# Kernel tuning notes

Measured on AMD Instinct MI355X. Metric: run time of the kernel, lower is better.

## Reference

```python
import jax, jax.numpy as jnp
import numpy as np

N = 100_000      # nodes
E = 3_200_000    # edges (avg degree 32)
DIM = 512        # input feature dim
HID = 16         # GCNConv hidden dim (fixed in __init__)
C = 64           # n_classes
DROP_P = 0.5     # F.dropout default


def _gcn_conv(x, W, b, row, col, deg_inv_sqrt, n_nodes):
    """PyG GCNConv: h = x@W; out[j] += norm_ij * h[i]; out += b.
    row/col already include self-loops; deg_inv_sqrt precomputed."""
    h = x @ W                                  # [N, out]
    norm = deg_inv_sqrt[row] * deg_inv_sqrt[col]  # [E+N]
    msg = h[row] * norm[:, None]               # gather + scale
    out = jax.ops.segment_sum(msg, col, num_segments=n_nodes)
    return out + b


def setup_inputs() -> dict:
    key = jax.random.key(0)
    k = jax.random.split(key, 6)
    x = jax.random.normal(k[0], (N, DIM), dtype=jnp.float32)
    edge_index = jax.random.randint(k[1], (2, E), 0, N, dtype=jnp.int32)
    W1 = jax.random.normal(k[2], (DIM, HID), dtype=jnp.float32) * (1.0 / np.sqrt(DIM))
    b1 = jnp.zeros((HID,), dtype=jnp.float32)
    W2 = jax.random.normal(k[3], (HID, C), dtype=jnp.float32) * (1.0 / np.sqrt(HID))
    b2 = jnp.zeros((C,), dtype=jnp.float32)
    return {"x": x, "edge_index": edge_index, "W1": W1, "b1": b1, "W2": W2, "b2": b2}


def reference(x, edge_index, W1, b1, W2, b2):
    n = x.shape[0]
    loops = jnp.arange(n, dtype=edge_index.dtype)
    row = jnp.concatenate([edge_index[0], loops])  # sources (with self-loops)
    col = jnp.concatenate([edge_index[1], loops])  # targets (with self-loops)
    # symmetric normalization: deg over targets with unit edge weight
    deg = jax.ops.segment_sum(jnp.ones_like(col, dtype=x.dtype), col, num_segments=n)
    deg_inv_sqrt = jnp.where(deg > 0, jax.lax.rsqrt(deg), 0.0)

    h = jax.nn.relu(_gcn_conv(x, W1, b1, row, col, deg_inv_sqrt, n))
    # F.dropout(x) -> p=0.5, training=True; deterministic fixed key
    keep = jax.random.bernoulli(jax.random.key(42), 1.0 - DROP_P, h.shape)
    h = jnp.where(keep, h / (1.0 - DROP_P), 0.0)
    logits = _gcn_conv(h, W2, b2, row, col, deg_inv_sqrt, n)
    return jax.nn.log_softmax(logits, axis=1)
```

## Files before the change

### kernel.cpp

```cpp
#include <hip/hip_runtime.h>

#define NN    100000
#define NE    3200000
#define DIMK  512
#define HIDN  16
#define NCLS  64
#define NBUCK 391
#define NBLK  512
#define CHUNK 6250
#define BCAP  10240

__device__ __forceinline__ unsigned rotl32(unsigned x, int r){ return (x << r) | (x >> (32 - r)); }

__device__ __forceinline__ unsigned threefry_bits(unsigned i){
  const unsigned k0 = 0u, k1 = 42u;
  const unsigned k2 = 0x1BD11BDAu ^ k0 ^ k1;
  unsigned a = 0u + k0, b = i + k1;
#define TF_R(r) { a += b; b = rotl32(b, (r)); b ^= a; }
  TF_R(13) TF_R(15) TF_R(26) TF_R(6)  a += k1; b += k2 + 1u;
  TF_R(17) TF_R(29) TF_R(16) TF_R(24) a += k2; b += k0 + 2u;
  TF_R(13) TF_R(15) TF_R(26) TF_R(6)  a += k0; b += k1 + 3u;
  TF_R(17) TF_R(29) TF_R(16) TF_R(24) a += k1; b += k2 + 4u;
  TF_R(13) TF_R(15) TF_R(26) TF_R(6)  a += k2; b += k0 + 5u;
#undef TF_R
  return a ^ b;
}

__global__ __launch_bounds__(256) void kp1_hist(const int* __restrict__ col, int* __restrict__ M){
  __shared__ int h[NBUCK];
  const int blk = blockIdx.x, t = threadIdx.x;
  for (int q = t; q < NBUCK; q += 256) h[q] = 0;
  __syncthreads();
  const int e0 = blk * CHUNK;
  for (int i = t; i < CHUNK; i += 256)
    atomicAdd(&h[col[e0 + i] >> 8], 1);
  __syncthreads();
  for (int q = t; q < NBUCK; q += 256) M[blk * NBUCK + q] = h[q];
}

__global__ __launch_bounds__(512) void kp2_rowscan(int* __restrict__ M, int* __restrict__ btot){
  __shared__ int s[512];
  const int b = blockIdx.x, t = threadIdx.x;
  const int idx = t * NBUCK + b;
  int v = M[idx];
  int x = v;
  s[t] = x; __syncthreads();
  for (int d = 1; d < 512; d <<= 1){
    int y = (t >= d) ? s[t - d] : 0;
    __syncthreads();
    x += y; s[t] = x;
    __syncthreads();
  }
  M[idx] = x - v;
  if (t == 511) btot[b] = x;
}

__global__ __launch_bounds__(512) void kp2b_bscan(const int* __restrict__ btot, int* __restrict__ bbase){
  __shared__ int s[512];
  const int t = threadIdx.x;
  int v = (t < NBUCK) ? btot[t] : 0;
  int x = v;
  s[t] = x; __syncthreads();
  for (int d = 1; d < 512; d <<= 1){
    int y = (t >= d) ? s[t - d] : 0;
    __syncthreads();
    x += y; s[t] = x;
    __syncthreads();
  }
  if (t < NBUCK) bbase[t] = x - v;
  if (t == NBUCK - 1) bbase[NBUCK] = x;
}

__global__ __launch_bounds__(256) void kp3_scatter(const int* __restrict__ row, const int* __restrict__ col,
                                                   const int* __restrict__ M, const int* __restrict__ bbase,
                                                   unsigned* __restrict__ coarse){
  __shared__ int cur[NBUCK];
  const int blk = blockIdx.x, t = threadIdx.x;
  for (int q = t; q < NBUCK; q += 256) cur[q] = bbase[q] + M[blk * NBUCK + q];
  __syncthreads();
  const int e0 = blk * CHUNK;
  for (int i = t; i < CHUNK; i += 256){
    int c = col[e0 + i];
    int r = row[e0 + i];
    int p = atomicAdd(&cur[c >> 8], 1);
    coarse[p] = ((unsigned)(c & 255) << 17) | (unsigned)r;
  }
}

__global__ __launch_bounds__(1024) void kd_dis(const unsigned* __restrict__ coarse,
                                               const int* __restrict__ bbase,
                                               float* __restrict__ dis){
  __shared__ int cnt[256];
  const int b = blockIdx.x, t = threadIdx.x;
  if (t < 256) cnt[t] = 0;
  __syncthreads();
  const int base = bbase[b];
  const int nreg = bbase[b + 1] - base;
  for (int i = t; i < nreg; i += 1024)
    atomicAdd(&cnt[coarse[base + i] >> 17], 1);
  __syncthreads();
  if (t < 256){
    int n = (b << 8) + t;
    if (n < NN) dis[n] = rsqrtf((float)(cnt[t] + 1));
  }
}

__global__ __launch_bounds__(256) void k_gemm1(const float* __restrict__ x,
                                               const float* __restrict__ W1,
                                               const float* __restrict__ dis,
                                               _Float16* __restrict__ hs16){
  const int lane = threadIdx.x & 63;
  const int wid  = (blockIdx.x * blockDim.x + threadIdx.x) >> 6;
  const int nw   = (gridDim.x * blockDim.x) >> 6;
  const bool s5 = (lane & 32) != 0;
  const bool s4 = (lane & 16) != 0;
  const bool s3 = (lane & 8)  != 0;
  const bool s2 = (lane & 4)  != 0;

  float4 w4[8][4];
  const float4* W1v = (const float4*)W1;
#pragma unroll
  for (int k = 0; k < 8; ++k)
#pragma unroll
    for (int jj = 0; jj < 4; ++jj)
      w4[k][jj] = W1v[(lane * 8 + k) * 4 + jj];

  for (int n = wid; n < NN; n += nw){
    const float4* xp = (const float4*)(x + (size_t)n * DIMK + lane * 8);
    float4 xa = xp[0], xb = xp[1];
    float xv[8] = {xa.x, xa.y, xa.z, xa.w, xb.x, xb.y, xb.z, xb.w};
    float acc[16];
#pragma unroll
    for (int j = 0; j < 16; ++j) acc[j] = 0.f;
#pragma unroll
    for (int k = 0; k < 8; ++k){
      float xk = xv[k];
#pragma unroll
      for (int jj = 0; jj < 4; ++jj){
        acc[jj*4+0] = fmaf(xk, w4[k][jj].x, acc[jj*4+0]);
        acc[jj*4+1] = fmaf(xk, w4[k][jj].y, acc[jj*4+1]);
        acc[jj*4+2] = fmaf(xk, w4[k][jj].z, acc[jj*4+2]);
        acc[jj*4+3] = fmaf(xk, w4[k][jj].w, acc[jj*4+3]);
      }
    }
    float t8[8];
#pragma unroll
    for (int m = 0; m < 8; ++m){
      float keep = s5 ? acc[8+m] : acc[m];
      float give = s5 ? acc[m]   : acc[8+m];
      t8[m] = keep + __shfl_xor(give, 32, 64);
    }
    float t4[4];
#pragma unroll
    for (int m = 0; m < 4; ++m){
      float keep = s4 ? t8[4+m] : t8[m];
      float give = s4 ? t8[m]   : t8[4+m];
      t4[m] = keep + __shfl_xor(give, 16, 64);
    }
    float t2[2];
#pragma unroll
    for (int m = 0; m < 2; ++m){
      float keep = s3 ? t4[2+m] : t4[m];
      float give = s3 ? t4[m]   : t4[2+m];
      t2[m] = keep + __shfl_xor(give, 8, 64);
    }
    float keep = s2 ? t2[1] : t2[0];
    float give = s2 ? t2[0] : t2[1];
    float v = keep + __shfl_xor(give, 4, 64);
    v += __shfl_xor(v, 2, 64);
    v += __shfl_xor(v, 1, 64);
    float hv = __shfl(v, (lane & 15) * 4, 64);
    if (lane < 16) hs16[(size_t)n * HIDN + lane] = (_Float16)(hv * dis[n]);
  }
}

__global__ __launch_bounds__(1024) void k_sortagg1(const unsigned* __restrict__ coarse,
                                                   const int* __restrict__ bbase,
                                                   const _Float16* __restrict__ hs16,
                                                   const float* __restrict__ dis,
                                                   const float* __restrict__ b1,
                                                   int* __restrict__ csr,
                                                   int* __restrict__ dstart,
                                                   int* __restrict__ dcnt,
                                                   _Float16* __restrict__ h2s16){
  __shared__ int ldsCsr[BCAP];
  __shared__ int cnt[256], ofs[256], rk[256], s[256];
  const int b = blockIdx.x, t = threadIdx.x;
  const int base = bbase[b];
  const int nreg = min(bbase[b + 1] - base, BCAP);
  if (t < 256){ cnt[t] = 0; rk[t] = 0; }
  __syncthreads();
  for (int i = t; i < nreg; i += 1024)
    atomicAdd(&cnt[coarse[base + i] >> 17], 1);
  __syncthreads();
  int deg = 0, x = 0;
  if (t < 256){ deg = cnt[t]; x = deg; s[t] = x; }
  __syncthreads();
  for (int d = 1; d < 256; d <<= 1){
    int y = 0;
    if (t < 256 && t >= d) y = s[t - d];
    __syncthreads();
    if (t < 256){ x += y; s[t] = x; }
    __syncthreads();
  }
  if (t < 256) ofs[t] = x - deg;
  __syncthreads();
  for (int i = t; i < nreg; i += 1024){
    unsigned p = coarse[base + i];
    int l = p >> 17;
    int q = atomicAdd(&rk[l], 1);
    ldsCsr[ofs[l] + q] = (int)(p & 0x1FFFFu);
  }
  if (t < 256){
    int n = (b << 8) + t;
    if (n < NN){ dstart[n] = base + ofs[t]; dcnt[n] = cnt[t]; }
  }
  __syncthreads();
  for (int q = t; q < nreg; q += 1024) csr[base + q] = ldsCsr[q];
  const int g = t >> 4, j = t & 15;
  for (int d = g; d < 256; d += 64){
    const int n = (b << 8) + d;
    if (n >= NN) break;
    const int st = ofs[d], cn = cnt[d];
    float acc = 0.f;
    int i = 0;
    for (; i + 2 <= cn; i += 2){
      int r0 = ldsCsr[st + i];
      int r1 = ldsCsr[st + i + 1];
      float a0 = (float)hs16[r0 * HIDN + j];
      float a1 = (float)hs16[r1 * HIDN + j];
      acc += a0 + a1;
    }
    if (i < cn) acc += (float)hs16[ldsCsr[st + i] * HIDN + j];
    float dn = dis[n];
    float v = fmaf(dn, acc + (float)hs16[(size_t)n * HIDN + j], b1[j]);
    v = fmaxf(v, 0.f);
    unsigned bits = threefry_bits((unsigned)(n * HIDN + j));
    float kept = (bits & 0x80000000u) ? 0.f : v * 2.f;
    h2s16[(size_t)n * HIDN + j] = (_Float16)(kept * dn);
  }
}

__global__ __launch_bounds__(256) void k_agg2out(const int* __restrict__ csr,
                                                 const int* __restrict__ dstart,
                                                 const int* __restrict__ dcnt,
                                                 const _Float16* __restrict__ h2s16,
                                                 const float* __restrict__ dis,
                                                 const float* __restrict__ W2,
                                                 const float* __restrict__ b2,
                                                 float* __restrict__ out){
  const int lane = threadIdx.x & 63;
  const int wid  = (blockIdx.x * blockDim.x + threadIdx.x) >> 6;
  const int nw   = (gridDim.x * blockDim.x) >> 6;
  const int j  = lane & 15;
  const int c4 = lane >> 4;
  float wc[16];
#pragma unroll
  for (int k = 0; k < 16; ++k) wc[k] = W2[k * NCLS + lane];
  const float bb = b2[lane];
  for (int n = wid; n < NN; n += nw){
    const int start = dstart[n];
    const int end   = start + dcnt[n];
    float acc = 0.f;
    for (int base = start; base < end; base += 64){
      const int m = min(end - base, 64);
      int rv = (lane < m) ? csr[base + lane] : 0;
      const int itmax = (m + 3) >> 2;
      for (int it = 0; it < itmax; ++it){
        int e = it * 4 + c4;
        int r = __shfl(rv, e & 63, 64);
        if (e < m) acc += (float)h2s16[r * HIDN + j];
      }
    }
    acc += __shfl_xor(acc, 16, 64);
    acc += __shfl_xor(acc, 32, 64);
    float dn = dis[n];
    float aggj = dn * (acc + (float)h2s16[(size_t)n * HIDN + j]);
    float s = bb;
#pragma unroll
    for (int k = 0; k < 16; ++k) s = fmaf(__shfl(aggj, k, 64), wc[k], s);
    float m2 = s;
#pragma unroll
    for (int d = 32; d; d >>= 1) m2 = fmaxf(m2, __shfl_xor(m2, d, 64));
    float ex = __expf(s - m2);
    float sum = ex;
#pragma unroll
    for (int d = 32; d; d >>= 1) sum += __shfl_xor(sum, d, 64);
    out[(size_t)n * NCLS + lane] = (s - m2) - __logf(sum);
  }
}

extern "C" void kernel_launch(void* const* d_in, const int* in_sizes, int n_in,
                              void* d_out, int out_size, void* d_ws, size_t ws_size,
                              hipStream_t stream){
  const float* x  = (const float*)d_in[0];
  const int*   ei = (const int*)  d_in[1];
  const float* W1 = (const float*)d_in[2];
  const float* b1 = (const float*)d_in[3];
  const float* W2 = (const float*)d_in[4];
  const float* b2 = (const float*)d_in[5];
  float* out = (float*)d_out;
  const int* row = ei;
  const int* col = ei + NE;

  char* ws = (char*)d_ws;
  int*       M      = (int*)      (ws + 0);
  int*       btot   = (int*)      (ws + 800768);
  int*       bbase  = (int*)      (ws + 802368);
  int*       dstart = (int*)      (ws + 803968);
  int*       dcnt   = (int*)      (ws + 1203968);
  float*     dis    = (float*)    (ws + 1603968);
  int*       csr    = (int*)      (ws + 2003968);
  unsigned*  coarse = (unsigned*) (ws + 14803968);
  _Float16*  hs16   = (_Float16*) (ws + 27603968);
  _Float16*  h2s16  = (_Float16*) (ws + 30803968);

  kp1_hist   <<<NBLK, 256, 0, stream>>>(col, M);
  kp2_rowscan<<<NBUCK, 512, 0, stream>>>(M, btot);
  kp2b_bscan <<<1, 512, 0, stream>>>(btot, bbase);
  kp3_scatter<<<NBLK, 256, 0, stream>>>(row, col, M, bbase, coarse);
  kd_dis     <<<NBUCK, 1024, 0, stream>>>(coarse, bbase, dis);
  k_gemm1    <<<1024, 256, 0, stream>>>(x, W1, dis, hs16);
  k_sortagg1 <<<NBUCK, 1024, 0, stream>>>(coarse, bbase, hs16, dis, b1, csr, dstart, dcnt, h2s16);
  k_agg2out  <<<2048, 256, 0, stream>>>(csr, dstart, dcnt, h2s16, dis, W2, b2, out);
}
```

Baseline: 509.3 us.

## Drop global CSR; rebuild per-bucket CSR in LDS for second aggregation

Moves the degree prefix scan into the metadata kernel so dstart/dcnt are computed once. The global CSR array is no longer written. The second aggregation instead re-sorts the coarse bucket into LDS per block and aggregates there, then applies W2 and log-softmax from an LDS accumulator. This removes a 12.8MB CSR write and read, at the cost of repeating the LDS bucket sort and running the second layer with only 391 large blocks.

```diff
diff --git a/kernel.cpp b/kernel.cpp
--- a/kernel.cpp
+++ b/kernel.cpp
@@ -87,10 +87,12 @@
   }
 }
 
-__global__ __launch_bounds__(1024) void kd_dis(const unsigned* __restrict__ coarse,
-                                               const int* __restrict__ bbase,
-                                               float* __restrict__ dis){
-  __shared__ int cnt[256];
+__global__ __launch_bounds__(1024) void kd_meta(const unsigned* __restrict__ coarse,
+                                                const int* __restrict__ bbase,
+                                                int* __restrict__ dstart,
+                                                int* __restrict__ dcnt,
+                                                float* __restrict__ dis){
+  __shared__ int cnt[256], s[256];
   const int b = blockIdx.x, t = threadIdx.x;
   if (t < 256) cnt[t] = 0;
   __syncthreads();
@@ -99,9 +101,23 @@
   for (int i = t; i < nreg; i += 1024)
     atomicAdd(&cnt[coarse[base + i] >> 17], 1);
   __syncthreads();
+  int deg = 0, x = 0;
+  if (t < 256){ deg = cnt[t]; x = deg; s[t] = x; }
+  __syncthreads();
+  for (int d = 1; d < 256; d <<= 1){
+    int y = 0;
+    if (t < 256 && t >= d) y = s[t - d];
+    __syncthreads();
+    if (t < 256){ x += y; s[t] = x; }
+    __syncthreads();
+  }
   if (t < 256){
     int n = (b << 8) + t;
-    if (n < NN) dis[n] = rsqrtf((float)(cnt[t] + 1));
+    if (n < NN){
+      dstart[n] = base + (x - deg);
+      dcnt[n]   = deg;
+      dis[n]    = rsqrtf((float)(deg + 1));
+    }
   }
 }
 
@@ -176,34 +192,23 @@
 
 __global__ __launch_bounds__(1024) void k_sortagg1(const unsigned* __restrict__ coarse,
                                                    const int* __restrict__ bbase,
+                                                   const int* __restrict__ dstart,
+                                                   const int* __restrict__ dcnt,
                                                    const _Float16* __restrict__ hs16,
                                                    const float* __restrict__ dis,
                                                    const float* __restrict__ b1,
-                                                   int* __restrict__ csr,
-                                                   int* __restrict__ dstart,
-                                                   int* __restrict__ dcnt,
                                                    _Float16* __restrict__ h2s16){
   __shared__ int ldsCsr[BCAP];
-  __shared__ int cnt[256], ofs[256], rk[256], s[256];
+  __shared__ int ofs[256], cnt[256], rk[256];
   const int b = blockIdx.x, t = threadIdx.x;
   const int base = bbase[b];
   const int nreg = min(bbase[b + 1] - base, BCAP);
-  if (t < 256){ cnt[t] = 0; rk[t] = 0; }
-  __syncthreads();
-  for (int i = t; i < nreg; i += 1024)
-    atomicAdd(&cnt[coarse[base + i] >> 17], 1);
-  __syncthreads();
-  int deg = 0, x = 0;
-  if (t < 256){ deg = cnt[t]; x = deg; s[t] = x; }
-  __syncthreads();
-  for (int d = 1; d < 256; d <<= 1){
-    int y = 0;
-    if (t < 256 && t >= d) y = s[t - d];
-    __syncthreads();
-    if (t < 256){ x += y; s[t] = x; }
-    __syncthreads();
-  }
-  if (t < 256) ofs[t] = x - deg;
+  if (t < 256){
+    int n = (b << 8) + t;
+    rk[t] = 0;
+    if (n < NN){ ofs[t] = dstart[n] - base; cnt[t] = dcnt[n]; }
+    else       { ofs[t] = 0;               cnt[t] = 0; }
+  }
   __syncthreads();
   for (int i = t; i < nreg; i += 1024){
     unsigned p = coarse[base + i];
@@ -211,12 +216,7 @@
     int q = atomicAdd(&rk[l], 1);
     ldsCsr[ofs[l] + q] = (int)(p & 0x1FFFFu);
   }
-  if (t < 256){
-    int n = (b << 8) + t;
-    if (n < NN){ dstart[n] = base + ofs[t]; dcnt[n] = cnt[t]; }
-  }
-  __syncthreads();
-  for (int q = t; q < nreg; q += 1024) csr[base + q] = ldsCsr[q];
+  __syncthreads();
   const int g = t >> 4, j = t & 15;
   for (int d = g; d < 256; d += 64){
     const int n = (b << 8) + d;
@@ -241,51 +241,73 @@
   }
 }
 
-__global__ __launch_bounds__(256) void k_agg2out(const int* __restrict__ csr,
-                                                 const int* __restrict__ dstart,
-                                                 const int* __restrict__ dcnt,
-                                                 const _Float16* __restrict__ h2s16,
-                                                 const float* __restrict__ dis,
-                                                 const float* __restrict__ W2,
-                                                 const float* __restrict__ b2,
-                                                 float* __restrict__ out){
-  const int lane = threadIdx.x & 63;
-  const int wid  = (blockIdx.x * blockDim.x + threadIdx.x) >> 6;
-  const int nw   = (gridDim.x * blockDim.x) >> 6;
-  const int j  = lane & 15;
-  const int c4 = lane >> 4;
+__global__ __launch_bounds__(1024) void k_agg2b(const unsigned* __restrict__ coarse,
+                                                const int* __restrict__ bbase,
+                                                const int* __restrict__ dstart,
+                                                const int* __restrict__ dcnt,
+                                                const _Float16* __restrict__ h2s16,
+                                                const float* __restrict__ dis,
+                                                const float* __restrict__ W2,
+                                                const float* __restrict__ b2,
+                                                float* __restrict__ out){
+  __shared__ int ldsCsr[BCAP];
+  __shared__ int ofs[256], cnt[256], rk[256];
+  __shared__ float accT[256 * HIDN];
+  const int b = blockIdx.x, t = threadIdx.x;
+  const int base = bbase[b];
+  const int nreg = min(bbase[b + 1] - base, BCAP);
+  if (t < 256){
+    int n = (b << 8) + t;
+    rk[t] = 0;
+    if (n < NN){ ofs[t] = dstart[n] - base; cnt[t] = dcnt[n]; }
+    else       { ofs[t] = 0;               cnt[t] = 0; }
+  }
+  __syncthreads();
+  for (int i = t; i < nreg; i += 1024){
+    unsigned p = coarse[base + i];
+    int l = p >> 17;
+    int q = atomicAdd(&rk[l], 1);
+    ldsCsr[ofs[l] + q] = (int)(p & 0x1FFFFu);
+  }
+  __syncthreads();
+  const int g = t >> 4, j = t & 15;
+  for (int d = g; d < 256; d += 64){
+    const int n = (b << 8) + d;
+    float acc = 0.f;
+    if (n < NN){
+      const int st = ofs[d], cn = cnt[d];
+      int i = 0;
+      for (; i + 2 <= cn; i += 2){
+        int r0 = ldsCsr[st + i];
+        int r1 = ldsCsr[st + i + 1];
+        acc += (float)h2s16[r0 * HIDN + j] + (float)h2s16[r1 * HIDN + j];
+      }
+      if (i < cn) acc += (float)h2s16[ldsCsr[st + i] * HIDN + j];
+    }
+    accT[d * HIDN + j] = acc;
+  }
+  __syncthreads();
+  const int lane = t & 63, w = t >> 6;
   float wc[16];
 #pragma unroll
   for (int k = 0; k < 16; ++k) wc[k] = W2[k * NCLS + lane];
   const float bb = b2[lane];
-  for (int n = wid; n < NN; n += nw){
-    const int start = dstart[n];
-    const int end   = start + dcnt[n];
-    float acc = 0.f;
-    for (int base = start; base < end; base += 64){
-      const int m = min(end - base, 64);
-      int rv = (lane < m) ? csr[base + lane] : 0;
-      const int itmax = (m + 3) >> 2;
-      for (int it = 0; it < itmax; ++it){
-        int e = it * 4 + c4;
-        int r = __shfl(rv, e & 63, 64);
-        if (e < m) acc += (float)h2s16[r * HIDN + j];
-      }
-    }
-    acc += __shfl_xor(acc, 16, 64);
-    acc += __shfl_xor(acc, 32, 64);
+  for (int d = w; d < 256; d += 16){
+    int n = (b << 8) + d;
+    if (n >= NN) continue;
     float dn = dis[n];
-    float aggj = dn * (acc + (float)h2s16[(size_t)n * HIDN + j]);
+    int jl = lane & 15;
+    float aggj = dn * (accT[d * HIDN + jl] + (float)h2s16[(size_t)n * HIDN + jl]);
     float s = bb;
 #pragma unroll
     for (int k = 0; k < 16; ++k) s = fmaf(__shfl(aggj, k, 64), wc[k], s);
     float m2 = s;
 #pragma unroll
-    for (int d = 32; d; d >>= 1) m2 = fmaxf(m2, __shfl_xor(m2, d, 64));
+    for (int dd = 32; dd; dd >>= 1) m2 = fmaxf(m2, __shfl_xor(m2, dd, 64));
     float ex = __expf(s - m2);
     float sum = ex;
 #pragma unroll
-    for (int d = 32; d; d >>= 1) sum += __shfl_xor(sum, d, 64);
+    for (int dd = 32; dd; dd >>= 1) sum += __shfl_xor(sum, dd, 64);
     out[(size_t)n * NCLS + lane] = (s - m2) - __logf(sum);
   }
 }
@@ -310,17 +332,16 @@
   int*       dstart = (int*)      (ws + 803968);
   int*       dcnt   = (int*)      (ws + 1203968);
   float*     dis    = (float*)    (ws + 1603968);
-  int*       csr    = (int*)      (ws + 2003968);
-  unsigned*  coarse = (unsigned*) (ws + 14803968);
-  _Float16*  hs16   = (_Float16*) (ws + 27603968);
-  _Float16*  h2s16  = (_Float16*) (ws + 30803968);
+  unsigned*  coarse = (unsigned*) (ws + 2003968);
+  _Float16*  hs16   = (_Float16*) (ws + 14803968);
+  _Float16*  h2s16  = (_Float16*) (ws + 18003968);
 
   kp1_hist   <<<NBLK, 256, 0, stream>>>(col, M);
   kp2_rowscan<<<NBUCK, 512, 0, stream>>>(M, btot);
   kp2b_bscan <<<1, 512, 0, stream>>>(btot, bbase);
   kp3_scatter<<<NBLK, 256, 0, stream>>>(row, col, M, bbase, coarse);
-  kd_dis     <<<NBUCK, 1024, 0, stream>>>(coarse, bbase, dis);
+  kd_meta    <<<NBUCK, 1024, 0, stream>>>(coarse, bbase, dstart, dcnt, dis);
   k_gemm1    <<<1024, 256, 0, stream>>>(x, W1, dis, hs16);
-  k_sortagg1 <<<NBUCK, 1024, 0, stream>>>(coarse, bbase, hs16, dis, b1, csr, dstart, dcnt, h2s16);
-  k_agg2out  <<<2048, 256, 0, stream>>>(csr, dstart, dcnt, h2s16, dis, W2, b2, out);
-}
+  k_sortagg1 <<<NBUCK, 1024, 0, stream>>>(coarse, bbase, dstart, dcnt, hs16, dis, b1, h2s16);
+  k_agg2b    <<<NBUCK, 1024, 0, stream>>>(coarse, bbase, dstart, dcnt, h2s16, dis, W2, b2, out);
+}
```

Result: no change. 507.6 us (-0.3%).
